# Performance work log

Measured on AMD Instinct MI355X. Metric: run time of the kernel, lower is better.

Reference implementation:

```python
import jax, jax.numpy as jnp
import numpy as np

B, S, H, NH = 2, 2048, 1024, 16
HD = H // NH  # 64


def setup_inputs() -> dict:
    key = jax.random.key(0)
    ks = jax.random.split(key, 9)
    s = 1.0 / np.sqrt(H)
    d = {"x": jax.random.normal(ks[0], (B, S, H), jnp.float32)}
    for i, n in enumerate(["Wq", "Wk", "Wv", "Wo"]):
        d[n] = jax.random.normal(ks[1 + i], (H, H), jnp.float32) * s
    for i, n in enumerate(["bq", "bk", "bv", "bo"]):
        d[n] = jax.random.normal(ks[5 + i], (H,), jnp.float32) * s
    return d


def _heads(x, W, b):
    # torch nn.Linear: y = x @ W.T + b, then split heads -> (B, NH, S, HD)
    y = x @ W.T + b
    return y.reshape(B, S, NH, HD).transpose(0, 2, 1, 3)


def _tetra_channels(t):
    # tetrapoint vector [a, 1-a, a*(1-a), clamp(1-(a+(1-a)),0,1)] for a scalar slice t
    a = jax.nn.sigmoid(t)
    na = 1.0 - a
    neither = jnp.clip(1.0 - (a + na), 0.0, 1.0)
    return jnp.stack([a, na, a * na, neither], axis=-1)  # (..., 4)


def reference(x, Wq, bq, Wk, bk, Wv, bv, Wo, bo):
    Q = _heads(x, Wq, bq)  # (B, NH, S, HD)
    K = _heads(x, Wk, bk)
    V = _heads(x, Wv, bv)
    # Original indexes Q_tetrapoints[:, :, :, 0] on [B,NH,S,HD,4]: selects head-dim
    # slot 0 (resp. 2) and keeps the 4 tetrapoint channels -> (B, NH, S, 4).
    Qa = _tetra_channels(Q[..., 0])
    Ka = _tetra_channels(K[..., 0])
    Qb = _tetra_channels(Q[..., 2])
    Kb = _tetra_channels(K[..., 2])
    scores = (jnp.einsum('bhsc,bhtc->bhst', Qa, Ka) / np.sqrt(HD)
              + 0.1 * jnp.einsum('bhsc,bhtc->bhst', Qb, Kb))  # (B, NH, S, S)
    w = jax.nn.softmax(scores, axis=-1)
    out = jnp.einsum('bhst,bhtd->bhsd', w, V)  # (B, NH, S, HD)
    out = out.transpose(0, 2, 1, 3).reshape(B, S, H)
    return out @ Wo.T + bo
```

## Files before the change

kernel.cpp:

```cpp
#include <hip/hip_runtime.h>
#include <hip/hip_bf16.h>

#define SS 2048
#define HH 1024
#define NHH 16
#define HDD 64

using f32x4  = __attribute__((ext_vector_type(4))) float;
using bf16x8 = __attribute__((ext_vector_type(8))) short;

#if __has_builtin(__builtin_amdgcn_exp2f)
#define EXP2F __builtin_amdgcn_exp2f
#else
#define EXP2F exp2f
#endif

__device__ __forceinline__ unsigned short f2bf(float f) {
    unsigned u = __builtin_bit_cast(unsigned, f);
    unsigned r = u + 0x7FFFu + ((u >> 16) & 1u);
    return (unsigned short)(r >> 16);
}

__device__ __forceinline__ unsigned bfround(float f) {
    unsigned u = __builtin_bit_cast(unsigned, f);
    return u + 0x7FFFu + ((u >> 16) & 1u);
}
__device__ __forceinline__ unsigned pack2bf(float a, float b) {
    return __builtin_amdgcn_perm(bfround(b), bfround(a), 0x07060302u);
}
__device__ __forceinline__ unsigned pack2bf_trunc(float a, float b) {
    return __builtin_amdgcn_perm(__builtin_bit_cast(unsigned, b),
                                 __builtin_bit_cast(unsigned, a), 0x07060302u);
}

__device__ __forceinline__ void tetra(float t, float* c) {
    float a = 1.f / (1.f + __expf(-t));
    float na = 1.f - a;
    float nei = 1.f - (a + na);
    nei = fminf(fmaxf(nei, 0.f), 1.f);
    c[0] = a; c[1] = na; c[2] = a * na; c[3] = nei;
}

__device__ __forceinline__ void gll16(const unsigned short* g, unsigned short* l) {
    __builtin_amdgcn_global_load_lds(
        (const __attribute__((address_space(1))) unsigned int*)g,
        (__attribute__((address_space(3))) unsigned int*)l, 16, 0, 0);
}

__global__ __launch_bounds__(256) void cvt_kernel(
    const float* __restrict__ x, const float* __restrict__ Wv, const float* __restrict__ Wo,
    const float* __restrict__ Wq, const float* __restrict__ Wk,
    const float* __restrict__ bq, const float* __restrict__ bk,
    unsigned short* __restrict__ xb, unsigned short* __restrict__ Wvb, unsigned short* __restrict__ Wob,
    unsigned short* __restrict__ wselb, float* __restrict__ bselws)
{
    if (blockIdx.x >= 2048) {
        int n = blockIdx.x - 2048;
        int h = n >> 2, q = n & 3;
        int rowIdx = h * HDD + ((q & 1) ? 2 : 0);
        const float* src  = (q & 2) ? Wk : Wq;
        const float* bsrc = (q & 2) ? bk : bq;
        int t = threadIdx.x;
        float4 v = *(const float4*)(src + (size_t)rowIdx * HH + t * 4);
        uint2 pk;
        pk.x = pack2bf(v.x, v.y);
        pk.y = pack2bf(v.z, v.w);
        *(uint2*)(wselb + (size_t)n * HH + t * 4) = pk;
        if (t == 0) bselws[n] = bsrc[rowIdx];
        return;
    }
    size_t gid = (size_t)blockIdx.x * 256 + threadIdx.x;
    size_t base = gid * 8;
    {
        float4 a = *(const float4*)(x + base);
        float4 b = *(const float4*)(x + base + 4);
        uint4 pk;
        pk.x = pack2bf(a.x, a.y);
        pk.y = pack2bf(a.z, a.w);
        pk.z = pack2bf(b.x, b.y);
        pk.w = pack2bf(b.z, b.w);
        *(uint4*)(xb + base) = pk;
    }
    if (base < 1048576) {
        float4 a = *(const float4*)(Wv + base);
        float4 b = *(const float4*)(Wv + base + 4);
        uint4 pk;
        pk.x = pack2bf(a.x, a.y);
        pk.y = pack2bf(a.z, a.w);
        pk.z = pack2bf(b.x, b.y);
        pk.w = pack2bf(b.z, b.w);
        *(uint4*)(Wvb + base) = pk;
        a = *(const float4*)(Wo + base);
        b = *(const float4*)(Wo + base + 4);
        pk.x = pack2bf(a.x, a.y);
        pk.y = pack2bf(a.z, a.w);
        pk.z = pack2bf(b.x, b.y);
        pk.w = pack2bf(b.z, b.w);
        *(uint4*)(Wob + base) = pk;
    }
}

template<int OUT_MODE>
__device__ __forceinline__ void gemm_body(unsigned char* smem,
    const unsigned short* __restrict__ A, const unsigned short* __restrict__ Bw,
    const float* __restrict__ bias, void* __restrict__ Cout, int bx, int by)
{
    auto As = (unsigned short (*)[64])smem;
    auto Bs = (unsigned short (*)[64])(smem + 16384);
    int tid = threadIdx.x;
    int wave = tid >> 6, lane = tid & 63;
    int l15 = lane & 15, l16 = lane >> 4;
    int wm = wave >> 1, wn = wave & 1;
    int m0 = by * 128, n0 = bx * 64;

    int srow = tid >> 3, scol = (tid & 7) * 8;
    const unsigned short* Ag = A + (size_t)(m0 + srow) * HH + scol;
    const unsigned short* Bg = Bw + (size_t)(n0 + srow) * HH + scol;
    unsigned short* Asl = &As[srow][scol];
    unsigned short* Bsl = &Bs[srow][scol];

    f32x4 acc[4][2] = {};

    for (int k0 = 0; k0 < HH; k0 += 64) {
        __syncthreads();
        #pragma unroll
        for (int i = 0; i < 4; i++)
            gll16(Ag + (size_t)(i * 32) * HH + k0, Asl + i * 32 * 64);
        #pragma unroll
        for (int i = 0; i < 2; i++)
            gll16(Bg + (size_t)(i * 32) * HH + k0, Bsl + i * 32 * 64);
        __syncthreads();

        #pragma unroll
        for (int kk = 0; kk < 64; kk += 32) {
            bf16x8 af[4], bfr[2];
            #pragma unroll
            for (int mi = 0; mi < 4; mi++)
                af[mi] = *(const bf16x8*)&As[wm * 64 + mi * 16 + l15][kk + l16 * 8];
            #pragma unroll
            for (int ni = 0; ni < 2; ni++)
                bfr[ni] = *(const bf16x8*)&Bs[wn * 32 + ni * 16 + l15][kk + l16 * 8];
            #pragma unroll
            for (int mi = 0; mi < 4; mi++)
                #pragma unroll
                for (int ni = 0; ni < 2; ni++)
                    acc[mi][ni] = __builtin_amdgcn_mfma_f32_16x16x32_bf16(af[mi], bfr[ni], acc[mi][ni], 0, 0, 0);
        }
    }

    float bv[2];
    #pragma unroll
    for (int ni = 0; ni < 2; ni++)
        bv[ni] = bias[n0 + wn * 32 + ni * 16 + l15];

    #pragma unroll
    for (int mi = 0; mi < 4; mi++) {
        #pragma unroll
        for (int ni = 0; ni < 2; ni++) {
            int n = n0 + wn * 32 + ni * 16 + l15;
            if (OUT_MODE == 0) {
                #pragma unroll
                for (int r = 0; r < 4; r++) {
                    int m = m0 + wm * 64 + mi * 16 + l16 * 4 + r;
                    ((float*)Cout)[(size_t)m * HH + n] = acc[mi][ni][r] + bv[ni];
                }
            } else {
                int m = m0 + wm * 64 + mi * 16 + l16 * 4;
                int b = m >> 11, s = m & 2047;
                int h = n >> 6, d = n & 63;
                uint2 pk;
                pk.x = pack2bf(acc[mi][ni][0] + bv[ni], acc[mi][ni][1] + bv[ni]);
                pk.y = pack2bf(acc[mi][ni][2] + bv[ni], acc[mi][ni][3] + bv[ni]);
                *(uint2*)((unsigned short*)Cout + ((size_t)((b * NHH + h) * HDD + d)) * SS + s) = pk;
            }
        }
    }
}

__device__ __forceinline__ void qk_body(unsigned char* smem,
    const unsigned short* __restrict__ xb, const unsigned short* __restrict__ wselb,
    const float* __restrict__ bselws,
    unsigned short* __restrict__ qfb, unsigned short* __restrict__ kfb, int blk)
{
    auto xs = (unsigned short (*)[72])smem;
    auto ws = (unsigned short (*)[72])(smem + 4608);
    auto ys = (float (*)[68])(smem + 13824);
    int tid = threadIdx.x;
    int wave = tid >> 6, lane = tid & 63;
    int l15 = lane & 15, l16 = lane >> 4;
    int m0 = blk * 32;
    int n0w = wave * 16;

    int xr = tid >> 3, xseg = (tid & 7) * 8;
    int wr = tid >> 2, wseg = (tid & 3) * 16;
    const unsigned short* xp = xb + (size_t)(m0 + xr) * HH + xseg;
    const unsigned short* wp = wselb + (size_t)wr * HH + wseg;

    f32x4 acc[2] = {};

    uint4 xv  = *(const uint4*)(xp);
    uint4 wv0 = *(const uint4*)(wp);
    uint4 wv1 = *(const uint4*)(wp + 8);

    for (int k0 = 0; k0 < HH; k0 += 64) {
        __syncthreads();
        *(uint4*)&xs[xr][xseg] = xv;
        *(uint4*)&ws[wr][wseg]     = wv0;
        *(uint4*)&ws[wr][wseg + 8] = wv1;
        __syncthreads();

        int kn = (k0 + 64) & (HH - 1);
        uint4 nxv  = *(const uint4*)(xp + kn);
        uint4 nwv0 = *(const uint4*)(wp + kn);
        uint4 nwv1 = *(const uint4*)(wp + kn + 8);

        #pragma unroll
        for (int kk = 0; kk < 64; kk += 32) {
            bf16x8 bfr = *(const bf16x8*)&ws[n0w + l15][kk + l16 * 8];
            #pragma unroll
            for (int mi = 0; mi < 2; mi++) {
                bf16x8 af = *(const bf16x8*)&xs[mi * 16 + l15][kk + l16 * 8];
                acc[mi] = __builtin_amdgcn_mfma_f32_16x16x32_bf16(af, bfr, acc[mi], 0, 0, 0);
            }
        }
        xv = nxv; wv0 = nwv0; wv1 = nwv1;
    }

    float bias = bselws[n0w + l15];
    __syncthreads();
    #pragma unroll
    for (int mi = 0; mi < 2; mi++)
        #pragma unroll
        for (int r = 0; r < 4; r++)
            ys[mi * 16 + l16 * 4 + r][n0w + l15] = acc[mi][r] + bias;
    __syncthreads();

    #pragma unroll
    for (int pass = 0; pass < 2; pass++) {
        int ml = tid & 31;
        int h = (tid >> 5) + pass * 8;
        float4 y4 = *(const float4*)&ys[ml][h * 4];
        float qa[4], qb2[4], ka[4], kb2[4];
        tetra(y4.x, qa);
        tetra(y4.y, qb2);
        tetra(y4.z, ka);
        tetra(y4.w, kb2);
        int m = m0 + ml, b = m >> 11, s = m & 2047;
        size_t base = ((size_t)(b * NHH + h) * SS + s) * 8;
        const float sA = 0.18033688011112042f;
        const float sB = 0.14426950408889634f;
        uint4 qp, kp;
        qp.x = pack2bf(qa[0] * sA, qa[1] * sA);
        qp.y = pack2bf(qa[2] * sA, qa[3] * sA);
        qp.z = pack2bf(qb2[0] * sB, qb2[1] * sB);
        qp.w = pack2bf(qb2[2] * sB, qb2[3] * sB);
        kp.x = pack2bf(ka[0], ka[1]);
        kp.y = pack2bf(ka[2], ka[3]);
        kp.z = pack2bf(kb2[0], kb2[1]);
        kp.w = pack2bf(kb2[2], kb2[3]);
        *(uint4*)(qfb + base) = qp;
        *(uint4*)(kfb + base) = kp;
    }
}

__global__ __launch_bounds__(256) void fused_mid(
    const unsigned short* __restrict__ xb,
    const unsigned short* __restrict__ Wvb, const float* __restrict__ bv,
    unsigned short* __restrict__ Vt,
    const unsigned short* __restrict__ wselb, const float* __restrict__ bselws,
    unsigned short* __restrict__ qfb, unsigned short* __restrict__ kfb)
{
    __shared__ __align__(16) unsigned char smem[24576];
    int id = blockIdx.x;
    if (id < 512)
        gemm_body<2>(smem, xb, Wvb, bv, Vt, id & 15, id >> 4);
    else
        qk_body(smem, xb, wselb, bselws, qfb, kfb, id - 512);
}

__global__ __launch_bounds__(256) void gemm_out(
    const unsigned short* __restrict__ A, const unsigned short* __restrict__ Bw,
    const float* __restrict__ bias, float* __restrict__ Cout)
{
    __shared__ __align__(16) unsigned char smem[24576];
    gemm_body<0>(smem, A, Bw, bias, Cout, blockIdx.x, blockIdx.y);
}

__global__ __launch_bounds__(256) void attn_mfma(
    const unsigned short* __restrict__ qfb, const unsigned short* __restrict__ kfb,
    const unsigned short* __restrict__ Vt, unsigned short* __restrict__ attnb)
{
    __shared__ __align__(16) unsigned char lds[32768];

    int tid = threadIdx.x;
    int wave = tid >> 6, lane = tid & 63;
    int l15 = lane & 15, l16 = lane >> 4;
    int l7 = l15 & 7;

    int L = blockIdx.x + (blockIdx.y << 4);
    int logical = ((L & 7) << 6) + (L >> 3);
    int bh = logical >> 4, qblk = logical & 15;
    int b = bh >> 4, h = bh & 15;
    int s0 = qblk * 128 + wave * 32;

    bf16x8 qA = {0,0,0,0,0,0,0,0}, qB = {0,0,0,0,0,0,0,0};
    if (l16 == 0) {
        qA = *(const bf16x8*)(qfb + ((size_t)bh * SS + s0 + l15) * 8);
        qB = *(const bf16x8*)(qfb + ((size_t)bh * SS + s0 + 16 + l15) * 8);
    }

    const short oneb = 0x3F80;
    bf16x8 ones = {oneb,oneb,oneb,oneb,oneb,oneb,oneb,oneb};

    const unsigned short* kfA = kfb + ((size_t)bh * SS + l15) * 8;
    int vd = tid >> 2, vr = tid & 3;
    const unsigned short* vsrc = Vt + ((size_t)bh * HDD + vd) * SS + vr * 16;

    unsigned char* vrow = lds + vd * 128;
    int sw0 = ((vr * 2)     ^ (vd & 7)) << 4;
    int sw1 = ((vr * 2 + 1) ^ (vd & 7)) << 4;
    unsigned char* psw = lds + 16384 + wave * 4096;

    f32x4 acc[2][4] = {};
    f32x4 accl[2] = {};

    {
        uint4 t0a = *(const uint4*)(vsrc);
        uint4 t0b = *(const uint4*)(vsrc + 8);
        *(uint4*)(vrow + sw0) = t0a;
        *(uint4*)(vrow + sw1) = t0b;
    }
    uint4 sv0 = *(const uint4*)(vsrc + 64);
    uint4 sv1 = *(const uint4*)(vsrc + 64 + 8);
    bf16x8 kfr[4];
    #pragma unroll
    for (int tb = 0; tb < 4; tb++)
        kfr[tb] = *(const bf16x8*)(kfA + (size_t)(tb * 16) * 8);

    for (int it = 0; it < 32; it++) {
        int t0 = it << 6;
        __syncthreads();

        int nb = (it + 1) & 1;
        *(uint4*)(vrow + nb * 8192 + sw0) = sv0;
        *(uint4*)(vrow + nb * 8192 + sw1) = sv1;

        int tv = (t0 + 128) & (SS - 1);
        uint4 nv0 = *(const uint4*)(vsrc + tv);
        uint4 nv1 = *(const uint4*)(vsrc + tv + 8);
        int tkf = (t0 + 64) & (SS - 1);
        bf16x8 nkf[4];
        #pragma unroll
        for (int tb = 0; tb < 4; tb++)
            nkf[tb] = *(const bf16x8*)(kfA + (size_t)(tkf + tb * 16) * 8);

        #pragma unroll
        for (int g = 0; g < 2; g++) {
            bf16x8 qf = g ? qB : qA;
            #pragma unroll
            for (int tb = 0; tb < 4; tb++) {
                f32x4 sc = {};
                sc = __builtin_amdgcn_mfma_f32_16x16x32_bf16(kfr[tb], qf, sc, 0, 0, 0);
                uint2 pw;
                pw.x = pack2bf_trunc(EXP2F(sc[0]), EXP2F(sc[1]));
                pw.y = pack2bf_trunc(EXP2F(sc[2]), EXP2F(sc[3]));
                int qr = g * 16 + l15;
                int c  = (tb * 2 + (l16 >> 1)) ^ l7;
                *(uint2*)(psw + qr * 128 + c * 16 + (l16 & 1) * 8) = pw;
            }
        }

        int cb = it & 1;
        unsigned char* vbuf = lds + cb * 8192;
        __builtin_amdgcn_s_setprio(1);
        #pragma unroll
        for (int tk = 0; tk < 2; tk++) {
            int csw = ((tk * 4 + l16) ^ l7) << 4;
            bf16x8 apA = *(const bf16x8*)(psw + l15 * 128 + csw);
            bf16x8 apB = *(const bf16x8*)(psw + (16 + l15) * 128 + csw);
            accl[0] = __builtin_amdgcn_mfma_f32_16x16x32_bf16(apA, ones, accl[0], 0, 0, 0);
            accl[1] = __builtin_amdgcn_mfma_f32_16x16x32_bf16(apB, ones, accl[1], 0, 0, 0);
            #pragma unroll
            for (int nd = 0; nd < 4; nd++) {
                bf16x8 bv = *(const bf16x8*)(vbuf + (nd * 16 + l15) * 128 + csw);
                acc[0][nd] = __builtin_amdgcn_mfma_f32_16x16x32_bf16(apA, bv, acc[0][nd], 0, 0, 0);
                acc[1][nd] = __builtin_amdgcn_mfma_f32_16x16x32_bf16(apB, bv, acc[1][nd], 0, 0, 0);
            }
        }
        __builtin_amdgcn_s_setprio(0);

        sv0 = nv0; sv1 = nv1;
        #pragma unroll
        for (int tb = 0; tb < 4; tb++) kfr[tb] = nkf[tb];
    }

    #pragma unroll
    for (int g = 0; g < 2; g++) {
        #pragma unroll
        for (int r = 0; r < 4; r++) {
            float linv = 1.f / accl[g][r];
            int q = s0 + g * 16 + l16 * 4 + r;
            size_t row = (size_t)(b * SS + q) * HH + h * HDD;
            #pragma unroll
            for (int nd = 0; nd < 4; nd++)
                attnb[row + nd * 16 + l15] = f2bf(acc[g][nd][r] * linv);
        }
    }
}

extern "C" void kernel_launch(void* const* d_in, const int* in_sizes, int n_in,
                              void* d_out, int out_size, void* d_ws, size_t ws_size,
                              hipStream_t stream)
{
    const float* x  = (const float*)d_in[0];
    const float* Wq = (const float*)d_in[1];
    const float* Wk = (const float*)d_in[2];
    const float* Wv = (const float*)d_in[3];
    const float* Wo = (const float*)d_in[4];
    const float* bq = (const float*)d_in[5];
    const float* bk = (const float*)d_in[6];
    const float* bv = (const float*)d_in[7];
    const float* bo = (const float*)d_in[8];

    unsigned short* qfb   = (unsigned short*)d_ws;
    unsigned short* kfb   = qfb + 524288;
    unsigned short* xb    = kfb + 524288;
    unsigned short* attnb = xb;
    unsigned short* Wvb   = xb + 4194304;
    unsigned short* Wob   = Wvb + 1048576;
    unsigned short* Vt    = Wob + 1048576;
    unsigned short* wselb  = Vt + 4194304;
    float*          bselws = (float*)(wselb + 65536);

    cvt_kernel<<<2112, 256, 0, stream>>>(x, Wv, Wo, Wq, Wk, bq, bk, xb, Wvb, Wob, wselb, bselws);
    fused_mid<<<640, 256, 0, stream>>>(xb, Wvb, bv, Vt, wselb, bselws, qfb, kfb);
    attn_mfma<<<dim3(16, 32), 256, 0, stream>>>(qfb, kfb, Vt, attnb);
    gemm_out<<<dim3(16, 32), 256, 0, stream>>>(attnb, Wob, bo, (float*)d_out);
}
```

Before: 173.4 us.

## Double-buffer GEMM LDS tiles with XOR swizzle and XCD-aware block remap

The shared GEMM body now prefetches the next K tile into a second LDS buffer while MFMAs consume the current one, cutting one barrier per iteration. Global-to-LDS loads are reorganised per wave, and the column index is XOR-swizzled to avoid LDS bank conflicts. Block IDs in fused_mid and gemm_out are remapped so that neighbouring tiles land on the same XCD for L2 reuse. LDS per block doubles to 48 KB, which may lower occupancy.

```diff
diff --git a/kernel.cpp b/kernel.cpp
--- a/kernel.cpp
+++ b/kernel.cpp
@@ -105,47 +105,65 @@
     const unsigned short* __restrict__ A, const unsigned short* __restrict__ Bw,
     const float* __restrict__ bias, void* __restrict__ Cout, int bx, int by)
 {
-    auto As = (unsigned short (*)[64])smem;
-    auto Bs = (unsigned short (*)[64])(smem + 16384);
     int tid = threadIdx.x;
     int wave = tid >> 6, lane = tid & 63;
     int l15 = lane & 15, l16 = lane >> 4;
     int wm = wave >> 1, wn = wave & 1;
     int m0 = by * 128, n0 = bx * 64;
 
-    int srow = tid >> 3, scol = (tid & 7) * 8;
-    const unsigned short* Ag = A + (size_t)(m0 + srow) * HH + scol;
-    const unsigned short* Bg = Bw + (size_t)(n0 + srow) * HH + scol;
-    unsigned short* Asl = &As[srow][scol];
-    unsigned short* Bsl = &Bs[srow][scol];
+    int lrow = lane >> 3;
+    int lcolsw = ((lane & 7) ^ lrow) * 8;
+    const unsigned short* Ag = A + (size_t)(m0 + wave * 32 + lrow) * HH + lcolsw;
+    const unsigned short* Bg = Bw + (size_t)(n0 + wave * 16 + lrow) * HH + lcolsw;
 
     f32x4 acc[4][2] = {};
 
+    {
+        unsigned short* As = (unsigned short*)smem + (size_t)wave * 32 * 64;
+        unsigned short* Bs = (unsigned short*)(smem + 16384) + (size_t)wave * 16 * 64;
+        #pragma unroll
+        for (int i = 0; i < 4; i++)
+            gll16(Ag + (size_t)(i * 8) * HH, As + i * 8 * 64);
+        #pragma unroll
+        for (int i = 0; i < 2; i++)
+            gll16(Bg + (size_t)(i * 8) * HH, Bs + i * 8 * 64);
+    }
+    __syncthreads();
+
+    int swq = l15 & 7;
+    int cur = 0;
     for (int k0 = 0; k0 < HH; k0 += 64) {
-        __syncthreads();
-        #pragma unroll
-        for (int i = 0; i < 4; i++)
-            gll16(Ag + (size_t)(i * 32) * HH + k0, Asl + i * 32 * 64);
-        #pragma unroll
-        for (int i = 0; i < 2; i++)
-            gll16(Bg + (size_t)(i * 32) * HH + k0, Bsl + i * 32 * 64);
-        __syncthreads();
-
-        #pragma unroll
-        for (int kk = 0; kk < 64; kk += 32) {
+        if (k0 + 64 < HH) {
+            unsigned char* nb = smem + (cur ^ 1) * 24576;
+            unsigned short* As = (unsigned short*)nb + (size_t)wave * 32 * 64;
+            unsigned short* Bs = (unsigned short*)(nb + 16384) + (size_t)wave * 16 * 64;
+            #pragma unroll
+            for (int i = 0; i < 4; i++)
+                gll16(Ag + (size_t)(i * 8) * HH + k0 + 64, As + i * 8 * 64);
+            #pragma unroll
+            for (int i = 0; i < 2; i++)
+                gll16(Bg + (size_t)(i * 8) * HH + k0 + 64, Bs + i * 8 * 64);
+        }
+
+        unsigned char* cb = smem + cur * 24576;
+        #pragma unroll
+        for (int kk = 0; kk < 2; kk++) {
+            int csw = ((kk * 4 + l16) ^ swq) * 16;
             bf16x8 af[4], bfr[2];
             #pragma unroll
             for (int mi = 0; mi < 4; mi++)
-                af[mi] = *(const bf16x8*)&As[wm * 64 + mi * 16 + l15][kk + l16 * 8];
+                af[mi] = *(const bf16x8*)(cb + (wm * 64 + mi * 16 + l15) * 128 + csw);
             #pragma unroll
             for (int ni = 0; ni < 2; ni++)
-                bfr[ni] = *(const bf16x8*)&Bs[wn * 32 + ni * 16 + l15][kk + l16 * 8];
+                bfr[ni] = *(const bf16x8*)(cb + 16384 + (wn * 32 + ni * 16 + l15) * 128 + csw);
             #pragma unroll
             for (int mi = 0; mi < 4; mi++)
                 #pragma unroll
                 for (int ni = 0; ni < 2; ni++)
                     acc[mi][ni] = __builtin_amdgcn_mfma_f32_16x16x32_bf16(af[mi], bfr[ni], acc[mi][ni], 0, 0, 0);
         }
+        __syncthreads();
+        cur ^= 1;
     }
 
     float bv[2];
@@ -270,20 +288,26 @@
     const unsigned short* __restrict__ wselb, const float* __restrict__ bselws,
     unsigned short* __restrict__ qfb, unsigned short* __restrict__ kfb)
 {
-    __shared__ __align__(16) unsigned char smem[24576];
-    int id = blockIdx.x;
-    if (id < 512)
+    __shared__ __align__(16) unsigned char smem[49152];
+    int p = blockIdx.x;
+    if (p < 512) {
+        int id = (p & 7) * 64 + (p >> 3);
         gemm_body<2>(smem, xb, Wvb, bv, Vt, id & 15, id >> 4);
-    else
-        qk_body(smem, xb, wselb, bselws, qfb, kfb, id - 512);
+    } else {
+        int q = p - 512;
+        int id = (q & 7) * 16 + (q >> 3);
+        qk_body(smem, xb, wselb, bselws, qfb, kfb, id);
+    }
 }
 
 __global__ __launch_bounds__(256) void gemm_out(
     const unsigned short* __restrict__ A, const unsigned short* __restrict__ Bw,
     const float* __restrict__ bias, float* __restrict__ Cout)
 {
-    __shared__ __align__(16) unsigned char smem[24576];
-    gemm_body<0>(smem, A, Bw, bias, Cout, blockIdx.x, blockIdx.y);
+    __shared__ __align__(16) unsigned char smem[49152];
+    int p = blockIdx.x;
+    int id = (p & 7) * 64 + (p >> 3);
+    gemm_body<0>(smem, A, Bw, bias, Cout, id & 15, id >> 4);
 }
 
 __global__ __launch_bounds__(256) void attn_mfma(
@@ -435,5 +459,5 @@
     cvt_kernel<<<2112, 256, 0, stream>>>(x, Wv, Wo, Wq, Wk, bq, bk, xb, Wvb, Wob, wselb, bselws);
     fused_mid<<<640, 256, 0, stream>>>(xb, Wvb, bv, Vt, wselb, bselws, qfb, kfb);
     attn_mfma<<<dim3(16, 32), 256, 0, stream>>>(qfb, kfb, Vt, attnb);
-    gemm_out<<<dim3(16, 32), 256, 0, stream>>>(attnb, Wob, bo, (float*)d_out);
-}
+    gemm_out<<<512, 256, 0, stream>>>(attnb, Wob, bo, (float*)d_out);
+}
```

Result: faster. 158.0 us (-8.9%).
